# Kernel optimization log

Measured on AMD Instinct MI355X. Metric: run time of the kernel, lower is better.

The kernel has to match this reference:

```python
import jax, jax.numpy as jnp
import numpy as np

B, N, T, F, H, NH, E, R = 16, 100, 96, 26, 128, 4, 16, 8


def _ln(x, g, b, eps=1e-5):
    m = x.mean(-1, keepdims=True)
    v = ((x - m) ** 2).mean(-1, keepdims=True)
    return (x - m) / jnp.sqrt(v + eps) * g + b


def setup_inputs() -> dict:
    ks = iter(jax.random.split(jax.random.key(0), 64))

    def nrm(*shape):
        return jax.random.normal(next(ks), shape, jnp.float32) * 0.05

    z = lambda *s: jnp.zeros(s, jnp.float32)
    o = lambda *s: jnp.ones(s, jnp.float32)
    inp = {}
    inp['x'] = jax.random.normal(next(ks), (B, N, T, F), jnp.float32)
    A = jax.random.uniform(next(ks), (N, N), jnp.float32)
    inp['A_norm'] = A / A.sum(1, keepdims=True)
    inp['H_inc'] = (jax.random.uniform(next(ks), (N, E)) > 0.7).astype(jnp.float32).at[:, 0].set(1.0)
    inp['membership'] = jax.random.randint(next(ks), (N,), 0, R)
    inp['Wp'] = nrm(H, F); inp['bp'] = z(H)
    inp['g_p'] = o(H); inp['b_p'] = z(H)
    inp['Wqkv'] = nrm(3 * H, H); inp['bqkv'] = z(3 * H)
    inp['Wo'] = nrm(H, H); inp['bo'] = z(H)
    inp['g_a'] = o(H); inp['b_a'] = z(H)
    inp['Wih_f'] = nrm(4 * H, H); inp['Whh_f'] = nrm(4 * H, H)
    inp['bih_f'] = z(4 * H); inp['bhh_f'] = z(4 * H)
    inp['Wih_b'] = nrm(4 * H, H); inp['Whh_b'] = nrm(4 * H, H)
    inp['bih_b'] = z(4 * H); inp['bhh_b'] = z(4 * H)
    inp['Wtp'] = nrm(H, 2 * H); inp['btp'] = z(H)
    inp['Wn'] = nrm(H, H); inp['bn'] = z(H)
    inp['We'] = nrm(H, H); inp['be'] = z(H)
    inp['Wa'] = nrm(1, H); inp['ba'] = z(1)
    inp['g_g'] = o(H); inp['b_g'] = z(H)
    inp['Remb'] = nrm(R, H)
    inp['Wg'] = nrm(H, H); inp['bg'] = z(H)
    inp['Wf'] = nrm(H, 2 * H); inp['bf'] = z(H)
    inp['g_f'] = o(H); inp['b_f'] = z(H)
    inp['W1'] = nrm(H // 2, H); inp['b1'] = z(H // 2)
    inp['W2'] = nrm(1, H // 2); inp['b2'] = z(1)
    return inp


def reference(x, A_norm, H_inc, membership, Wp, bp, g_p, b_p, Wqkv, bqkv, Wo, bo,
              g_a, b_a, Wih_f, Whh_f, bih_f, bhh_f, Wih_b, Whh_b, bih_b, bhh_b,
              Wtp, btp, Wn, bn, We, be, Wa, ba, g_g, b_g, Remb, Wg, bg,
              Wf, bf, g_f, b_f, W1, b1, W2, b2):
    B_, N_, T_, F_ = x.shape
    H_ = Wp.shape[0]
    BN = B_ * N_
    # input_proj (dropout = identity in eval)
    h = jax.nn.relu(_ln(x.reshape(BN, T_, F_) @ Wp.T + bp, g_p, b_p))
    # temporal multi-head self-attention + residual + LN
    qkv = h @ Wqkv.T + bqkv
    q, k, v = jnp.split(qkv, 3, -1)
    dh = H_ // NH
    sh = lambda t: t.reshape(BN, T_, NH, dh).transpose(0, 2, 1, 3)
    q, k, v = sh(q), sh(k), sh(v)
    att = jax.nn.softmax(jnp.einsum('bhqd,bhkd->bhqk', q, k) / jnp.sqrt(jnp.float32(dh)), -1)
    ao = jnp.einsum('bhqk,bhkd->bhqd', att, v).transpose(0, 2, 1, 3).reshape(BN, T_, H_)
    h = _ln(ao @ Wo.T + bo + h, g_a, b_a)
    # bidirectional LSTM (PyTorch gate order i,f,g,o), take t = T-1
    def lstm_scan(seq, Wih, Whh, bih, bhh):
        def step(carry, xt):
            hp, cp = carry
            gates = xt @ Wih.T + bih + hp @ Whh.T + bhh
            i, f, g, o_ = jnp.split(gates, 4, -1)
            c = jax.nn.sigmoid(f) * cp + jax.nn.sigmoid(i) * jnp.tanh(g)
            hn = jax.nn.sigmoid(o_) * jnp.tanh(c)
            return (hn, c), hn
        z0 = jnp.zeros((seq.shape[1], H_), seq.dtype)
        _, ys = jax.lax.scan(step, (z0, z0), seq)
        return ys
    seq = h.transpose(1, 0, 2)  # (T, BN, H)
    y_f = lstm_scan(seq, Wih_f, Whh_f, bih_f, bhh_f)[-1]        # fwd hidden at t=T-1
    y_b = lstm_scan(seq[::-1], Wih_b, Whh_b, bih_b, bhh_b)[0]   # bwd hidden at t=T-1
    h_temporal = (jnp.concatenate([y_f, y_b], -1) @ Wtp.T + btp).reshape(B_, N_, H_)
    # spatial: HyperGAT (segment softmax over incident hyperedges) + GCN + region emb
    mask = H_inc > 0                        # (N, E)
    deg_e = H_inc.sum(0)                    # (E,)
    has_edge = mask.any(-1, keepdims=True)  # (N, 1)
    r_emb = Remb[membership]                # (N, H)

    def spatial(hb):
        npj = hb @ Wn.T + bn
        ee = (H_inc.T @ npj) / (deg_e[:, None] + 1e-8)
        ee = ee @ We.T + be                 # (E, H)
        sc = (ee @ Wa.T + ba)[:, 0]         # (E,)
        w = jax.nn.softmax(jnp.where(mask, sc[None, :], -1e9), -1)
        w = jnp.where(has_edge, w, 0.0)
        hb2 = _ln(w @ ee + hb, g_g, b_g)
        hg = jax.nn.relu((A_norm @ hb2) @ Wg.T + bg)
        return hb2 + hg + r_emb

    h_spatial = jax.vmap(spatial)(h_temporal)
    h_fused = jax.nn.relu(_ln(jnp.concatenate([h_temporal, h_spatial], -1) @ Wf.T + bf, g_f, b_f))
    pred = (jax.nn.relu(h_fused @ W1.T + b1) @ W2.T + b2)[..., 0]
    return pred, h_spatial, h_temporal
```

## Files before the change

kernel.cpp:

```cpp
#include <hip/hip_runtime.h>
#include <hip/hip_bf16.h>

typedef __hip_bfloat16 bf16;
typedef __attribute__((ext_vector_type(8))) short bf8v;
typedef __attribute__((ext_vector_type(4))) short s4v;
typedef __attribute__((ext_vector_type(4))) float f4v;

#define DEV __device__ __forceinline__

DEV float b2f(bf16 v){ return __bfloat162float(v); }
DEV bf16 f2b(float v){ return __float2bfloat16(v); }
DEV short f2bs(float v){ bf16 t = __float2bfloat16(v); return *reinterpret_cast<short*>(&t); }
DEV float s2f(short s){ return __uint_as_float(((unsigned int)(unsigned short)s) << 16); }
DEV float rcpf_(float x){ return __builtin_amdgcn_rcpf(x); }
DEV float sigf(float x){ return rcpf_(1.0f + __expf(-x)); }
DEV float tanhfast(float x){
  x = fminf(fmaxf(x, -15.0f), 15.0f);
  float e = __expf(-2.0f*x);
  return (1.0f - e)*rcpf_(1.0f + e);
}

DEV f4v mfma16(bf8v a, bf8v b, f4v c){
  return __builtin_amdgcn_mfma_f32_16x16x32_bf16(a, b, c, 0, 0, 0);
}

__global__ void k_detect(const unsigned int* __restrict__ xw, int* __restrict__ flag){
  __shared__ int found;
  if (threadIdx.x == 0) found = 0;
  __syncthreads();
  int local = 0;
  for (int i = threadIdx.x; i < 4096; i += 256){
    unsigned int u = xw[i];
    unsigned int e = (u >> 7) & 0xFF;
    if (e >= 0x90) local = 1;
  }
  if (local) atomicOr(&found, 1);
  __syncthreads();
  if (threadIdx.x == 0) flag[0] = found ? 0 : 1;
}

struct CArgs {
  const void* src[44];
  int n[44];
  int off[44];
};

__global__ void k_canon(CArgs a, const int* __restrict__ flag, bf16* __restrict__ dst){
  int id = blockIdx.y;
  int n = a.n[id];
  const void* s = a.src[id];
  bf16* d = dst + a.off[id];
  int stride = gridDim.x * blockDim.x;
  int i0 = blockIdx.x * blockDim.x + threadIdx.x;
  if (flag[0]){
    const bf16* sb = (const bf16*)s;
    for (int i = i0; i < n; i += stride) d[i] = sb[i];
  } else {
    const float* sf = (const float*)s;
    for (int i = i0; i < n; i += stride) d[i] = f2b(sf[i]);
  }
}

__global__ void k_prep(const bf16* __restrict__ Wp, const bf16* __restrict__ An,
                       bf16* __restrict__ Wpp, bf16* __restrict__ Anp,
                       bf16* __restrict__ htp, bf16* __restrict__ hb2p){
  int stride = gridDim.x * blockDim.x;
  bf16 zero = f2b(0.0f);
  for (int i = blockIdx.x*blockDim.x + threadIdx.x; i < 477184; i += stride){
    if (i < 4096){
      int row = i >> 5, col = i & 31;
      Wpp[i] = (col < 26) ? Wp[row*26 + col] : zero;
    } else if (i < 18432){
      int j = i - 4096;
      int row = j >> 7, col = j & 127;
      Anp[j] = (row < 100 && col < 100) ? An[row*100 + col] : zero;
    } else if (i < 247808){
      htp[i - 18432] = zero;
    } else {
      hb2p[i - 247808] = zero;
    }
  }
}

__global__ __launch_bounds__(256) void k_inproj(const bf16* __restrict__ x,
    const bf16* __restrict__ Wpp, const bf16* __restrict__ bp,
    const bf16* __restrict__ gp, const bf16* __restrict__ bbp,
    bf16* __restrict__ h0){
  int blk = blockIdx.x, tid = threadIdx.x;
  int w = tid >> 6, lane = tid & 63, l15 = lane & 15, quad = lane >> 4;
  __shared__ __align__(16) short flat[3328];
  __shared__ __align__(16) short xt[128*40];
  {
    const uint4* src = (const uint4*)(x + blk*3328);
    uint4* dst = (uint4*)flat;
    for (int u = tid; u < 416; u += 256) dst[u] = src[u];
  }
  __syncthreads();
  for (int i = tid; i < 5120; i += 256){
    int row = i/40, col = i - row*40;
    xt[i] = (col < 26) ? flat[row*26 + col] : (short)0;
  }
  __syncthreads();
  int m0 = w*32;
  bf8v a[2];
  #pragma unroll
  for (int m = 0; m < 2; ++m)
    a[m] = *reinterpret_cast<const bf8v*>(xt + (m0 + m*16 + l15)*40 + quad*8);
  f4v acc[2][8];
  for (int n = 0; n < 8; ++n){
    bf8v bb = *reinterpret_cast<const bf8v*>(Wpp + (n*16 + l15)*32 + quad*8);
    #pragma unroll
    for (int m = 0; m < 2; ++m){
      f4v z = {0.f,0.f,0.f,0.f};
      acc[m][n] = mfma16(a[m], bb, z);
    }
  }
  #pragma unroll
  for (int m = 0; m < 2; ++m){
    int rowbase = blk*128 + m0 + m*16;
    float sm[4], sq[4];
    #pragma unroll
    for (int r = 0; r < 4; ++r){ sm[r] = 0.f; sq[r] = 0.f; }
    #pragma unroll
    for (int n = 0; n < 8; ++n){
      int col = n*16 + l15;
      float bv = b2f(bp[col]);
      #pragma unroll
      for (int r = 0; r < 4; ++r){
        float v = acc[m][n][r] + bv;
        acc[m][n][r] = v;
        sm[r] += v; sq[r] += v*v;
      }
    }
    #pragma unroll
    for (int mask = 1; mask < 16; mask <<= 1)
      #pragma unroll
      for (int r = 0; r < 4; ++r){
        sm[r] += __shfl_xor(sm[r], mask);
        sq[r] += __shfl_xor(sq[r], mask);
      }
    float mean[4], rs[4];
    #pragma unroll
    for (int r = 0; r < 4; ++r){
      mean[r] = sm[r]*(1.0f/128.0f);
      float var = fmaxf(sq[r]*(1.0f/128.0f) - mean[r]*mean[r], 0.0f);
      rs[r] = rsqrtf(var + 1e-5f);
    }
    #pragma unroll
    for (int n = 0; n < 8; ++n){
      int col = n*16 + l15;
      float gv = b2f(gp[col]), bv = b2f(bbp[col]);
      #pragma unroll
      for (int r = 0; r < 4; ++r){
        float y = fmaxf((acc[m][n][r] - mean[r])*rs[r]*gv + bv, 0.0f);
        h0[(rowbase + quad*4 + r)*128 + col] = f2b(y);
      }
    }
  }
}

__global__ __launch_bounds__(256) void k_attn(const bf16* __restrict__ h0,
    const bf16* __restrict__ Wqkv, const bf16* __restrict__ bqkv,
    bf16* __restrict__ attno){
  int bn = blockIdx.x;
  int tid = threadIdx.x;
  int w = tid >> 6;
  int lane = tid & 63;
  int l15 = lane & 15, quad = lane >> 4;

  __shared__ __align__(16) short h0s[96*136];
  __shared__ __align__(16) short v_sh[4][32*104];
  __shared__ __align__(16) short scr[4][16*40];

  {
    const uint4* src = (const uint4*)(h0 + bn*12288);
    uint4* dst = (uint4*)h0s;
    for (int u = tid; u < 1536; u += 256){
      int r = u >> 4, c = u & 15;
      dst[r*17 + c] = src[u];
    }
  }
  __syncthreads();

  short* vp = v_sh[w];
  short* sw = scr[w];
  const float scl = 0.17677669529663687f;

  bf8v aq[6], bk[6];
  for (int m = 0; m < 6; ++m){
    bf8v a[4];
    #pragma unroll
    for (int kt = 0; kt < 4; ++kt)
      a[kt] = *reinterpret_cast<const bf8v*>(h0s + (m*16 + l15)*136 + kt*32 + quad*8);
    #pragma unroll
    for (int n0 = 0; n0 < 32; n0 += 16){
      int rq = w*32 + n0 + l15;
      bf8v b[4];
      #pragma unroll
      for (int kt = 0; kt < 4; ++kt)
        b[kt] = *reinterpret_cast<const bf8v*>(Wqkv + rq*128 + kt*32 + quad*8);
      float bias = b2f(bqkv[rq]);
      f4v acc = {0.f,0.f,0.f,0.f};
      #pragma unroll
      for (int kt = 0; kt < 4; ++kt) acc = mfma16(a[kt], b[kt], acc);
      #pragma unroll
      for (int r = 0; r < 4; ++r)
        sw[(quad*4 + r)*40 + n0 + l15] = f2bs((acc[r] + bias)*scl);
    }
    asm volatile("s_waitcnt lgkmcnt(0)" ::: "memory");
    aq[m] = *reinterpret_cast<const bf8v*>(sw + l15*40 + quad*8);
  }
  for (int m = 0; m < 6; ++m){
    bf8v a[4];
    #pragma unroll
    for (int kt = 0; kt < 4; ++kt)
      a[kt] = *reinterpret_cast<const bf8v*>(h0s + (m*16 + l15)*136 + kt*32 + quad*8);
    #pragma unroll
    for (int n0 = 0; n0 < 32; n0 += 16){
      int rq = 128 + w*32 + n0 + l15;
      bf8v b[4];
      #pragma unroll
      for (int kt = 0; kt < 4; ++kt)
        b[kt] = *reinterpret_cast<const bf8v*>(Wqkv + rq*128 + kt*32 + quad*8);
      float bias = b2f(bqkv[rq]);
      f4v acc = {0.f,0.f,0.f,0.f};
      #pragma unroll
      for (int kt = 0; kt < 4; ++kt) acc = mfma16(a[kt], b[kt], acc);
      #pragma unroll
      for (int r = 0; r < 4; ++r)
        sw[(quad*4 + r)*40 + n0 + l15] = f2bs(acc[r] + bias);
    }
    asm volatile("s_waitcnt lgkmcnt(0)" ::: "memory");
    bk[m] = *reinterpret_cast<const bf8v*>(sw + l15*40 + quad*8);
  }
  for (int m = 0; m < 6; ++m){
    bf8v a[4];
    #pragma unroll
    for (int kt = 0; kt < 4; ++kt)
      a[kt] = *reinterpret_cast<const bf8v*>(h0s + (m*16 + l15)*136 + kt*32 + quad*8);
    #pragma unroll
    for (int n0 = 0; n0 < 32; n0 += 16){
      int rq = 256 + w*32 + n0 + l15;
      bf8v b[4];
      #pragma unroll
      for (int kt = 0; kt < 4; ++kt)
        b[kt] = *reinterpret_cast<const bf8v*>(Wqkv + rq*128 + kt*32 + quad*8);
      float bias = b2f(bqkv[rq]);
      f4v acc = {0.f,0.f,0.f,0.f};
      #pragma unroll
      for (int kt = 0; kt < 4; ++kt) acc = mfma16(a[kt], b[kt], acc);
      s4v vs;
      #pragma unroll
      for (int r = 0; r < 4; ++r) vs[r] = f2bs(acc[r] + bias);
      *reinterpret_cast<s4v*>(vp + (n0 + l15)*104 + m*16 + quad*4) = vs;
    }
  }
  __syncthreads();

  short* pp = h0s + w*1664;

  for (int m = 0; m < 6; ++m){
    f4v s[6];
    #pragma unroll
    for (int n = 0; n < 6; ++n){
      f4v z = {0.f,0.f,0.f,0.f};
      s[n] = mfma16(aq[m], bk[n], z);
    }
    float mr[4], sr[4];
    #pragma unroll
    for (int r = 0; r < 4; ++r){
      float m0 = fmaxf(fmaxf(s[0][r], s[1][r]), fmaxf(s[2][r], s[3][r]));
      mr[r] = fmaxf(m0, fmaxf(s[4][r], s[5][r]));
    }
    #pragma unroll
    for (int mask = 1; mask < 16; mask <<= 1)
      #pragma unroll
      for (int r = 0; r < 4; ++r) mr[r] = fmaxf(mr[r], __shfl_xor(mr[r], mask));
    #pragma unroll
    for (int r = 0; r < 4; ++r) sr[r] = 0.0f;
    #pragma unroll
    for (int n = 0; n < 6; ++n)
      #pragma unroll
      for (int r = 0; r < 4; ++r){
        float p = __expf(s[n][r] - mr[r]);
        s[n][r] = p;
        sr[r] += p;
      }
    #pragma unroll
    for (int mask = 1; mask < 16; mask <<= 1)
      #pragma unroll
      for (int r = 0; r < 4; ++r) sr[r] += __shfl_xor(sr[r], mask);
    #pragma unroll
    for (int n = 0; n < 6; ++n)
      #pragma unroll
      for (int r = 0; r < 4; ++r)
        pp[(quad*4 + r)*104 + n*16 + l15] = f2bs(s[n][r]);
    asm volatile("s_waitcnt lgkmcnt(0)" ::: "memory");
    f4v o0 = {0.f,0.f,0.f,0.f}, o1 = {0.f,0.f,0.f,0.f};
    #pragma unroll
    for (int ksi = 0; ksi < 3; ++ksi){
      bf8v ap  = *reinterpret_cast<const bf8v*>(pp + l15*104 + ksi*32 + quad*8);
      bf8v bv0 = *reinterpret_cast<const bf8v*>(vp + l15*104 + ksi*32 + quad*8);
      bf8v bv1 = *reinterpret_cast<const bf8v*>(vp + (16 + l15)*104 + ksi*32 + quad*8);
      o0 = mfma16(ap, bv0, o0);
      o1 = mfma16(ap, bv1, o1);
    }
    #pragma unroll
    for (int r = 0; r < 4; ++r){
      float inv = 1.0f/sr[r];
      int row = bn*96 + m*16 + quad*4 + r;
      attno[row*128 + w*32 + l15]      = f2b(o0[r]*inv);
      attno[row*128 + w*32 + 16 + l15] = f2b(o1[r]*inv);
    }
  }
}

__global__ __launch_bounds__(256) void k_oproj(const bf16* __restrict__ attno,
    const bf16* __restrict__ h0, const bf16* __restrict__ Wo,
    const bf16* __restrict__ bo, const bf16* __restrict__ ga,
    const bf16* __restrict__ ba_, bf16* __restrict__ h1){
  int rt = blockIdx.x;
  int tid = threadIdx.x;
  int w = tid >> 6, lane = tid & 63;
  int l15 = lane & 15, quad = lane >> 4;
  __shared__ __align__(16) short atile[128*136];
  {
    const uint4* src = (const uint4*)(attno + rt*16384);
    uint4* dst = (uint4*)atile;
    for (int u = tid; u < 2048; u += 256){
      int r = u >> 4, c = u & 15;
      dst[r*17 + c] = src[u];
    }
  }
  __syncthreads();
  int m0 = w*32;
  bf8v a[2][4];
  #pragma unroll
  for (int m = 0; m < 2; ++m)
    #pragma unroll
    for (int ksi = 0; ksi < 4; ++ksi)
      a[m][ksi] = *reinterpret_cast<const bf8v*>(atile + (m0 + m*16 + l15)*136 + ksi*32 + quad*8);
  f4v acc[2][8];
  #pragma unroll
  for (int m = 0; m < 2; ++m)
    #pragma unroll
    for (int n = 0; n < 8; ++n) acc[m][n] = (f4v){0.f,0.f,0.f,0.f};
  for (int n = 0; n < 8; ++n){
    int G = n*16 + l15;
    bf8v b[4];
    #pragma unroll
    for (int ksi = 0; ksi < 4; ++ksi)
      b[ksi] = *reinterpret_cast<const bf8v*>(Wo + G*128 + ksi*32 + quad*8);
    #pragma unroll
    for (int m = 0; m < 2; ++m)
      #pragma unroll
      for (int ksi = 0; ksi < 4; ++ksi)
        acc[m][n] = mfma16(a[m][ksi], b[ksi], acc[m][n]);
  }
  #pragma unroll
  for (int m = 0; m < 2; ++m){
    int rowbase = rt*128 + m0 + m*16;
    #pragma unroll
    for (int n = 0; n < 8; ++n){
      int col = n*16 + l15;
      float bia = b2f(bo[col]);
      #pragma unroll
      for (int r = 0; r < 4; ++r)
        acc[m][n][r] += bia + b2f(h0[(rowbase + quad*4 + r)*128 + col]);
    }
    float sm[4], sq[4];
    #pragma unroll
    for (int r = 0; r < 4; ++r){ sm[r] = 0.f; sq[r] = 0.f; }
    #pragma unroll
    for (int n = 0; n < 8; ++n)
      #pragma unroll
      for (int r = 0; r < 4; ++r){
        float v = acc[m][n][r];
        sm[r] += v; sq[r] += v*v;
      }
    #pragma unroll
    for (int mask = 1; mask < 16; mask <<= 1)
      #pragma unroll
      for (int r = 0; r < 4; ++r){
        sm[r] += __shfl_xor(sm[r], mask);
        sq[r] += __shfl_xor(sq[r], mask);
      }
    float mean[4], rs[4];
    #pragma unroll
    for (int r = 0; r < 4; ++r){
      mean[r] = sm[r]*(1.0f/128.0f);
      float var = fmaxf(sq[r]*(1.0f/128.0f) - mean[r]*mean[r], 0.0f);
      rs[r] = rsqrtf(var + 1e-5f);
    }
    #pragma unroll
    for (int n = 0; n < 8; ++n){
      int col = n*16 + l15;
      float gv = b2f(ga[col]), bv = b2f(ba_[col]);
      #pragma unroll
      for (int r = 0; r < 4; ++r){
        float y = (acc[m][n][r] - mean[r])*rs[r]*gv + bv;
        h1[(rowbase + quad*4 + r)*128 + col] = f2b(y);
      }
    }
  }
}

__global__ __launch_bounds__(512,1) void k_lstm(const bf16* __restrict__ Whh,
    const bf16* __restrict__ Wih, const bf16* __restrict__ bih,
    const bf16* __restrict__ bhh, const bf16* __restrict__ h1,
    const bf16* __restrict__ Wihb, const bf16* __restrict__ bihb,
    const bf16* __restrict__ bhhb, const bf16* __restrict__ Wtp,
    const bf16* __restrict__ btp, bf16* __restrict__ ht_pad,
    const int* __restrict__ flag, bf16* __restrict__ outb,
    float* __restrict__ outf){
  int bn0 = blockIdx.x * 16;
  int tid = threadIdx.x;
  int w = tid >> 6, lane = tid & 63;
  int l15 = lane & 15, quad = lane >> 4;
  __shared__ __align__(16) short hbuf[2][16*136];
  __shared__ __align__(16) short xbuf[2][16*136];
  __shared__ __align__(16) short ycat[16*264];

  bf8v whh[4][4], wih[4][4];
  float bias[4];
  #pragma unroll
  for (int role = 0; role < 4; ++role){
    int G = role*128 + w*16 + l15;
    #pragma unroll
    for (int kt = 0; kt < 4; ++kt){
      whh[role][kt] = *reinterpret_cast<const bf8v*>(Whh + G*128 + kt*32 + quad*8);
      wih[role][kt] = *reinterpret_cast<const bf8v*>(Wih + G*128 + kt*32 + quad*8);
    }
    bias[role] = b2f(bih[G]) + b2f(bhh[G]);
  }
  const uint4* h1u4 = (const uint4*)h1;
  int srow = tid >> 4, scol = tid & 15;

  for (int i = tid; i < 16*136; i += 512) hbuf[0][i] = 0;
  if (tid < 256)
    ((uint4*)xbuf[0])[srow*17 + scol] = h1u4[((bn0 + srow)*96 + 0)*16 + scol];
  f4v c0 = {0.f,0.f,0.f,0.f};
  uint4 xpre;
  if (tid < 256) xpre = h1u4[((bn0 + srow)*96 + 1)*16 + scol];
  __syncthreads();

  f4v accx[4];
  {
    bf8v ax[4];
    #pragma unroll
    for (int kt = 0; kt < 4; ++kt)
      ax[kt] = *reinterpret_cast<const bf8v*>(xbuf[0] + l15*136 + kt*32 + quad*8);
    #pragma unroll
    for (int role = 0; role < 4; ++role){
      f4v z = {0.f,0.f,0.f,0.f};
      #pragma unroll
      for (int kt = 0; kt < 4; ++kt) z = mfma16(ax[kt], wih[role][kt], z);
      accx[role] = z;
    }
  }
  if (tid < 256) ((uint4*)xbuf[1])[srow*17 + scol] = xpre;
  if (tid < 256) xpre = h1u4[((bn0 + srow)*96 + 2)*16 + scol];
  __syncthreads();

  for (int t = 0; t < 96; ++t){
    int cur = t & 1, nxt = cur ^ 1;
    bf8v ah[4], axn[4];
    #pragma unroll
    for (int kt = 0; kt < 4; ++kt){
      ah[kt]  = *reinterpret_cast<const bf8v*>(hbuf[cur] + l15*136 + kt*32 + quad*8);
      axn[kt] = *reinterpret_cast<const bf8v*>(xbuf[nxt] + l15*136 + kt*32 + quad*8);
    }
    f4v acc[4];
    #pragma unroll
    for (int role = 0; role < 4; ++role){
      f4v z = accx[role];
      #pragma unroll
      for (int kt = 0; kt < 4; ++kt) z = mfma16(ah[kt], whh[role][kt], z);
      acc[role] = z;
    }
    #pragma unroll
    for (int role = 0; role < 4; ++role){
      f4v z = {0.f,0.f,0.f,0.f};
      #pragma unroll
      for (int kt = 0; kt < 4; ++kt) z = mfma16(axn[kt], wih[role][kt], z);
      accx[role] = z;
    }
    float hreg[4];
    #pragma unroll
    for (int r = 0; r < 4; ++r){
      float i_ = acc[0][r] + bias[0];
      float f_ = acc[1][r] + bias[1];
      float g_ = acc[2][r] + bias[2];
      float o_ = acc[3][r] + bias[3];
      float c  = sigf(f_)*c0[r] + sigf(i_)*tanhfast(g_);
      hreg[r]  = sigf(o_)*tanhfast(c);
      c0[r] = c;
    }
    #pragma unroll
    for (int r = 0; r < 4; ++r)
      hbuf[nxt][(quad*4 + r)*136 + w*16 + l15] = f2bs(hreg[r]);
    if (tid < 256){
      ((uint4*)xbuf[cur])[srow*17 + scol] = xpre;
      int tl = (t + 3 < 96) ? t + 3 : 95;
      xpre = h1u4[((bn0 + srow)*96 + tl)*16 + scol];
    }
    __syncthreads();
  }
  for (int idx = tid; idx < 2048; idx += 512){
    int r = idx >> 7, d = idx & 127;
    ycat[r*264 + d] = hbuf[0][r*136 + d];
  }
  {
    bf8v ax[4];
    #pragma unroll
    for (int kt = 0; kt < 4; ++kt)
      ax[kt] = *reinterpret_cast<const bf8v*>(xbuf[0] + l15*136 + kt*32 + quad*8);
    int col = w*16 + l15;
    f4v gi = {0.f,0.f,0.f,0.f}, gg = {0.f,0.f,0.f,0.f}, go = {0.f,0.f,0.f,0.f};
    #pragma unroll
    for (int kt = 0; kt < 4; ++kt){
      gi = mfma16(ax[kt], *reinterpret_cast<const bf8v*>(Wihb + col*128 + kt*32 + quad*8), gi);
      gg = mfma16(ax[kt], *reinterpret_cast<const bf8v*>(Wihb + (256 + col)*128 + kt*32 + quad*8), gg);
      go = mfma16(ax[kt], *reinterpret_cast<const bf8v*>(Wihb + (384 + col)*128 + kt*32 + quad*8), go);
    }
    float bi = b2f(bihb[col])       + b2f(bhhb[col]);
    float bg = b2f(bihb[256 + col]) + b2f(bhhb[256 + col]);
    float bo = b2f(bihb[384 + col]) + b2f(bhhb[384 + col]);
    #pragma unroll
    for (int r = 0; r < 4; ++r){
      float c  = sigf(gi[r] + bi) * tanhfast(gg[r] + bg);
      float yb = sigf(go[r] + bo) * tanhfast(c);
      ycat[(quad*4 + r)*264 + 128 + col] = f2bs(yb);
    }
  }
  __syncthreads();
  {
    int col = w*16 + l15;
    f4v z = {0.f,0.f,0.f,0.f};
    #pragma unroll
    for (int kt = 0; kt < 8; ++kt){
      bf8v a = *reinterpret_cast<const bf8v*>(ycat + l15*264 + kt*32 + quad*8);
      bf8v bb = *reinterpret_cast<const bf8v*>(Wtp + col*256 + kt*32 + quad*8);
      z = mfma16(a, bb, z);
    }
    float bt = b2f(btp[col]);
    #pragma unroll
    for (int r = 0; r < 4; ++r){
      int rowg = bn0 + quad*4 + r;
      float v = z[r] + bt;
      int bb_ = rowg/100, nn = rowg - bb_*100;
      ht_pad[(bb_*112 + nn)*128 + col] = f2b(v);
      int oi = 206400 + rowg*128 + col;
      if (flag[0]) outb[oi] = f2b(v); else outf[oi] = v;
    }
  }
}

__global__ __launch_bounds__(512,1) void k_spat1(
    const bf16* __restrict__ ht_pad, const bf16* __restrict__ Hinc,
    const bf16* __restrict__ Wn, const bf16* __restrict__ bn_,
    const bf16* __restrict__ We, const bf16* __restrict__ be,
    const bf16* __restrict__ Wa, const bf16* __restrict__ ba,
    const bf16* __restrict__ gg_, const bf16* __restrict__ bg_,
    bf16* __restrict__ hb2g){
  int b = blockIdx.x, tid = threadIdx.x;
  int w = tid >> 6, lane = tid & 63, l15 = lane & 15, quad = lane >> 4;
  __shared__ __align__(16) short htb[112*136];
  __shared__ __align__(16) short mtile[16*136];
  __shared__ float HincS[1600];
  __shared__ float wts[1600];
  __shared__ float eeS[16*128];
  __shared__ float scE[16], degS[16], part[128];

  {
    const uint4* src = (const uint4*)(ht_pad + b*14336);
    uint4* dst = (uint4*)htb;
    for (int u = tid; u < 1792; u += 512){
      int r = u >> 4, c = u & 15;
      dst[r*17 + c] = src[u];
    }
  }
  for (int i = tid; i < 1600; i += 512) HincS[i] = b2f(Hinc[i]);
  __syncthreads();
  if (tid < 16){
    float s = 0.0f;
    for (int n = 0; n < 100; ++n) s += HincS[n*16 + tid];
    degS[tid] = s;
  }
  __syncthreads();
  for (int it = 0; it < 4; ++it){
    int idx = tid + it*512;
    int e = idx >> 7, d = idx & 127;
    float s = 0.0f;
    for (int n = 0; n < 100; ++n)
      s += HincS[n*16 + e] * s2f(htb[n*136 + d]);
    mtile[e*136 + d] = f2bs(s * rcpf_(degS[e] + 1e-8f));
  }
  __syncthreads();
  {
    bf8v a[4];
    #pragma unroll
    for (int kt = 0; kt < 4; ++kt)
      a[kt] = *reinterpret_cast<const bf8v*>(mtile + l15*136 + kt*32 + quad*8);
    int col = w*16 + l15;
    f4v z = {0.f,0.f,0.f,0.f};
    #pragma unroll
    for (int kt = 0; kt < 4; ++kt)
      z = mfma16(a[kt], *reinterpret_cast<const bf8v*>(Wn + col*128 + kt*32 + quad*8), z);
    float bnv = b2f(bn_[col]);
    __syncthreads();
    #pragma unroll
    for (int r = 0; r < 4; ++r){
      int e = quad*4 + r;
      float ratio = degS[e] * rcpf_(degS[e] + 1e-8f);
      mtile[e*136 + col] = f2bs(z[r] + bnv*ratio);
    }
  }
  __syncthreads();
  {
    bf8v a[4];
    #pragma unroll
    for (int kt = 0; kt < 4; ++kt)
      a[kt] = *reinterpret_cast<const bf8v*>(mtile + l15*136 + kt*32 + quad*8);
    int col = w*16 + l15;
    f4v z = {0.f,0.f,0.f,0.f};
    #pragma unroll
    for (int kt = 0; kt < 4; ++kt)
      z = mfma16(a[kt], *reinterpret_cast<const bf8v*>(We + col*128 + kt*32 + quad*8), z);
    float bev = b2f(be[col]);
    #pragma unroll
    for (int r = 0; r < 4; ++r)
      eeS[(quad*4 + r)*128 + col] = z[r] + bev;
  }
  __syncthreads();
  if (tid < 128){
    int e = tid >> 3, j = tid & 7;
    float s = 0.0f;
    for (int d = j*16; d < j*16 + 16; ++d)
      s += eeS[e*128 + d] * b2f(Wa[d]);
    part[tid] = s;
  }
  __syncthreads();
  if (tid < 16){
    float s = b2f(ba[0]);
    for (int j = 0; j < 8; ++j) s += part[tid*8 + j];
    scE[tid] = s;
  }
  __syncthreads();
  if (tid < 100){
    float sc[16], mx = -1e30f;
    for (int e = 0; e < 16; ++e){
      sc[e] = (HincS[tid*16 + e] > 0.0f) ? scE[e] : -1e30f;
      mx = fmaxf(mx, sc[e]);
    }
    float sum = 0.0f, tmp[16];
    for (int e = 0; e < 16; ++e){
      tmp[e] = (sc[e] > -1e29f) ? __expf(sc[e] - mx) : 0.0f;
      sum += tmp[e];
    }
    float inv = (sum > 0.0f) ? rcpf_(sum) : 0.0f;
    for (int e = 0; e < 16; ++e) wts[tid*16 + e] = tmp[e]*inv;
  }
  __syncthreads();
  for (int it = 0; it < 13; ++it){
    int n = it*8 + w;
    if (n < 100){
      int d0 = lane*2;
      float s0 = s2f(htb[n*136 + d0]);
      float s1 = s2f(htb[n*136 + d0 + 1]);
      for (int e = 0; e < 16; ++e){
        float wv = wts[n*16 + e];
        s0 += wv * eeS[e*128 + d0];
        s1 += wv * eeS[e*128 + d0 + 1];
      }
      float sum = s0 + s1, sq = s0*s0 + s1*s1;
      #pragma unroll
      for (int mask = 1; mask < 64; mask <<= 1){
        sum += __shfl_xor(sum, mask);
        sq  += __shfl_xor(sq, mask);
      }
      float mean = sum*(1.0f/128.0f);
      float var = fmaxf(sq*(1.0f/128.0f) - mean*mean, 0.0f);
      float rs = rsqrtf(var + 1e-5f);
      float y0 = (s0 - mean)*rs*b2f(gg_[d0])     + b2f(bg_[d0]);
      float y1 = (s1 - mean)*rs*b2f(gg_[d0 + 1]) + b2f(bg_[d0 + 1]);
      hb2g[b*14336 + n*128 + d0]     = f2b(y0);
      hb2g[b*14336 + n*128 + d0 + 1] = f2b(y1);
    }
  }
}

__global__ __launch_bounds__(512,1) void k_spat2(
    const bf16* __restrict__ hb2g, const bf16* __restrict__ Anp,
    const bf16* __restrict__ Wg, const bf16* __restrict__ bgc,
    const bf16* __restrict__ Remb, const int* __restrict__ mem,
    const bf16* __restrict__ ht_pad,
    const bf16* __restrict__ Wf, const bf16* __restrict__ bf_,
    const bf16* __restrict__ gf, const bf16* __restrict__ b_f,
    const bf16* __restrict__ W1, const bf16* __restrict__ b1,
    const bf16* __restrict__ W2, const bf16* __restrict__ b2,
    const int* __restrict__ flag, bf16* __restrict__ outb,
    float* __restrict__ outf){
  int b = blockIdx.x, tid = threadIdx.x;
  int w = tid >> 6, lane = tid & 63, l15 = lane & 15, quad = lane >> 4;
  __shared__ __align__(16) short regA[128*136];
  __shared__ __align__(16) short regB[112*136];

  for (int i = tid; i < 128*136; i += 512) regA[i] = 0;
  __syncthreads();
  {
    int c0 = w*16;
    bf8v bw[4];
    #pragma unroll
    for (int kt = 0; kt < 4; ++kt)
      bw[kt] = *reinterpret_cast<const bf8v*>(Wg + (c0 + l15)*128 + kt*32 + quad*8);
    for (int m = 0; m < 7; ++m){
      f4v z = {0.f,0.f,0.f,0.f};
      #pragma unroll
      for (int kt = 0; kt < 4; ++kt){
        bf8v a = *reinterpret_cast<const bf8v*>(hb2g + b*14336 + (m*16 + l15)*128 + kt*32 + quad*8);
        z = mfma16(a, bw[kt], z);
      }
      s4v vs;
      #pragma unroll
      for (int r = 0; r < 4; ++r) vs[r] = f2bs(z[r]);
      *reinterpret_cast<s4v*>(regA + (c0 + l15)*136 + m*16 + quad*4) = vs;
    }
  }
  __syncthreads();
  {
    int c0 = w*16;
    for (int m = 0; m < 7; ++m){
      f4v z = {0.f,0.f,0.f,0.f};
      #pragma unroll
      for (int kt = 0; kt < 4; ++kt){
        bf8v a  = *reinterpret_cast<const bf8v*>(Anp + (m*16 + l15)*128 + kt*32 + quad*8);
        bf8v bb = *reinterpret_cast<const bf8v*>(regA + (c0 + l15)*136 + kt*32 + quad*8);
        z = mfma16(a, bb, z);
      }
      #pragma unroll
      for (int r = 0; r < 4; ++r){
        int row = m*16 + quad*4 + r, col = c0 + l15;
        if (row < 100){
          float v = fmaxf(z[r] + b2f(bgc[col]), 0.0f);
          float o = b2f(hb2g[b*14336 + row*128 + col]) + v
                  + b2f(Remb[mem[row]*128 + col]);
          int oi = 1600 + (b*100 + row)*128 + col;
          if (flag[0]) outb[oi] = f2b(o); else outf[oi] = o;
          regB[row*136 + col] = f2bs(o);
        } else {
          regB[row*136 + col] = 0;
        }
      }
    }
  }
  __syncthreads();
  if (w < 7){
    int m = w;
    f4v acc[8];
    for (int n = 0; n < 8; ++n){
      f4v z = {0.f,0.f,0.f,0.f};
      #pragma unroll
      for (int kt = 0; kt < 4; ++kt){
        bf8v a  = *reinterpret_cast<const bf8v*>(ht_pad + b*14336 + (m*16 + l15)*128 + kt*32 + quad*8);
        bf8v bb = *reinterpret_cast<const bf8v*>(Wf + (n*16 + l15)*256 + kt*32 + quad*8);
        z = mfma16(a, bb, z);
      }
      #pragma unroll
      for (int kt = 0; kt < 4; ++kt){
        bf8v a  = *reinterpret_cast<const bf8v*>(regB + (m*16 + l15)*136 + kt*32 + quad*8);
        bf8v bb = *reinterpret_cast<const bf8v*>(Wf + (n*16 + l15)*256 + 128 + kt*32 + quad*8);
        z = mfma16(a, bb, z);
      }
      acc[n] = z;
    }
    float sm[4], sq[4];
    #pragma unroll
    for (int r = 0; r < 4; ++r){ sm[r] = 0.f; sq[r] = 0.f; }
    #pragma unroll
    for (int n = 0; n < 8; ++n){
      int col = n*16 + l15;
      float bv = b2f(bf_[col]);
      #pragma unroll
      for (int r = 0; r < 4; ++r){
        float v = acc[n][r] + bv;
        acc[n][r] = v;
        sm[r] += v; sq[r] += v*v;
      }
    }
    #pragma unroll
    for (int mask = 1; mask < 16; mask <<= 1)
      #pragma unroll
      for (int r = 0; r < 4; ++r){
        sm[r] += __shfl_xor(sm[r], mask);
        sq[r] += __shfl_xor(sq[r], mask);
      }
    #pragma unroll
    for (int r = 0; r < 4; ++r){
      float mean = sm[r]*(1.0f/128.0f);
      float var = fmaxf(sq[r]*(1.0f/128.0f) - mean*mean, 0.0f);
      float rs = rsqrtf(var + 1e-5f);
      #pragma unroll
      for (int n = 0; n < 8; ++n){
        int col = n*16 + l15;
        float y = fmaxf((acc[n][r] - mean)*rs*b2f(gf[col]) + b2f(b_f[col]), 0.0f);
        regA[(m*16 + quad*4 + r)*136 + col] = f2bs(y);
      }
    }
  }
  __syncthreads();
  if (w < 7){
    int m = w;
    for (int n = 0; n < 4; ++n){
      f4v z = {0.f,0.f,0.f,0.f};
      #pragma unroll
      for (int kt = 0; kt < 4; ++kt){
        bf8v a  = *reinterpret_cast<const bf8v*>(regA + (m*16 + l15)*136 + kt*32 + quad*8);
        bf8v bb = *reinterpret_cast<const bf8v*>(W1 + (n*16 + l15)*128 + kt*32 + quad*8);
        z = mfma16(a, bb, z);
      }
      #pragma unroll
      for (int r = 0; r < 4; ++r){
        int row = m*16 + quad*4 + r, col = n*16 + l15;
        regB[row*72 + col] = f2bs(fmaxf(z[r] + b2f(b1[col]), 0.0f));
      }
    }
  }
  __syncthreads();
  if (tid < 100){
    float s = b2f(b2[0]);
    for (int d = 0; d < 64; ++d)
      s += s2f(regB[tid*72 + d]) * b2f(W2[d]);
    int oi = b*100 + tid;
    if (flag[0]) outb[oi] = f2b(s); else outf[oi] = s;
  }
}


extern "C" void kernel_launch(void* const* d_in, const int* in_sizes, int n_in,
                              void* d_out, int out_size, void* d_ws, size_t ws_size,
                              hipStream_t stream){
  (void)n_in; (void)out_size; (void)ws_size;
  const int* mem = (const int*)d_in[3];

  CArgs ca;
  int coff[43];
  int nf = 0;
  long long off = 0;
  for (int i = 0; i < 43; ++i){
    if (i == 3){ coff[i] = -1; continue; }
    coff[i] = (int)off;
    ca.src[nf] = d_in[i];
    ca.n[nf]   = in_sizes[i];
    ca.off[nf] = (int)off;
    ++nf;
    off += (long long)((in_sizes[i] + 7) & ~7);
  }
  char* ws = (char*)d_ws;
  bf16* canon = (bf16*)ws;
  long long canonBytes = ((off*2 + 255)/256)*256;
  int* flag = (int*)(ws + canonBytes);
  long long base = canonBytes + 256;

  #define C(i) (canon + coff[i])
  const bf16* A_norm = C(1);
  const bf16* Hinc   = C(2);
  const bf16* Wp  = C(4);  const bf16* bp  = C(5);
  const bf16* g_p = C(6);  const bf16* b_p = C(7);
  const bf16* Wqkv= C(8);  const bf16* bqkv= C(9);
  const bf16* Wo  = C(10); const bf16* bo  = C(11);
  const bf16* g_a = C(12); const bf16* b_a = C(13);
  const bf16* Wih_f = C(14); const bf16* Whh_f = C(15);
  const bf16* bih_f = C(16); const bf16* bhh_f = C(17);
  const bf16* Wih_b = C(18);
  const bf16* bih_b = C(20); const bf16* bhh_b = C(21);
  const bf16* Wtp = C(22); const bf16* btp = C(23);
  const bf16* Wn  = C(24); const bf16* bn_ = C(25);
  const bf16* We  = C(26); const bf16* be  = C(27);
  const bf16* Wa  = C(28); const bf16* ba  = C(29);
  const bf16* g_g = C(30); const bf16* b_g = C(31);
  const bf16* Remb= C(32);
  const bf16* Wg  = C(33); const bf16* bg  = C(34);
  const bf16* Wf  = C(35); const bf16* bff = C(36);
  const bf16* g_f = C(37); const bf16* b_f = C(38);
  const bf16* W1  = C(39); const bf16* b1  = C(40);
  const bf16* W2  = C(41); const bf16* b2  = C(42);
  const bf16* xc  = C(0);
  #undef C

  bf16*  outb = (bf16*)d_out;
  float* outf = (float*)d_out;
  bf16*  h1     = (bf16*)(ws + base);
  bf16*  h0     = (bf16*)(ws + base + 39321600LL);
  bf16*  attno  = (bf16*)(ws + base + 78643200LL);
  bf16*  Wpp    = (bf16*)(ws + base + 196608000LL);
  bf16*  An_pad = (bf16*)(ws + base + 196616192LL);
  bf16*  ht_pad = (bf16*)(ws + base + 196644864LL);
  bf16*  hb2g   = (bf16*)(ws + base + 197103616LL);

  k_detect<<<1, 256, 0, stream>>>((const unsigned int*)d_in[0], flag);
  k_canon <<<dim3(64, nf), 256, 0, stream>>>(ca, flag, canon);
  k_prep  <<<1024, 256, 0, stream>>>(Wp, A_norm, Wpp, An_pad, ht_pad, hb2g);
  k_inproj<<<1200, 256, 0, stream>>>(xc, Wpp, bp, g_p, b_p, h0);
  k_attn  <<<1600, 256, 0, stream>>>(h0, Wqkv, bqkv, attno);
  k_oproj <<<1200, 256, 0, stream>>>(attno, h0, Wo, bo, g_a, b_a, h1);
  k_lstm  <<<100,  512, 0, stream>>>(Whh_f, Wih_f, bih_f, bhh_f, h1,
                                     Wih_b, bih_b, bhh_b, Wtp, btp, ht_pad,
                                     flag, outb, outf);
  k_spat1 <<<16,   512, 0, stream>>>(ht_pad, Hinc, Wn, bn_, We, be, Wa, ba,
                                     g_g, b_g, hb2g);
  k_spat2 <<<16,   512, 0, stream>>>(hb2g, An_pad, Wg, bg, Remb, mem, ht_pad,
                                     Wf, bff, g_f, b_f, W1, b1, W2, b2,
                                     flag, outb, outf);
}
```

Before: 514.7 us.

## Fuse input projection, self-attention and output projection into one kernel per sequence

Merges the three kernels (input projection + LayerNorm, multi-head temporal attention, output projection + residual + LayerNorm) into a single kernel with one block per (b,n) sequence. The intermediate h0 and attention outputs stay in shared memory, so the global round trips for h0 and attno and two launches go away. V fragments are also preloaded into registers before the score loop. The cost is higher LDS use and register pressure per block, which may lower occupancy, and the projection phases use only 6 row tiles across 4 waves, leaving some waves idle.

```diff
diff --git a/kernel.cpp b/kernel.cpp
--- a/kernel.cpp
+++ b/kernel.cpp
@@ -82,42 +82,38 @@
   }
 }
 
-__global__ __launch_bounds__(256) void k_inproj(const bf16* __restrict__ x,
+__global__ __launch_bounds__(256) void k_fat(const bf16* __restrict__ x,
     const bf16* __restrict__ Wpp, const bf16* __restrict__ bp,
     const bf16* __restrict__ gp, const bf16* __restrict__ bbp,
-    bf16* __restrict__ h0){
-  int blk = blockIdx.x, tid = threadIdx.x;
+    const bf16* __restrict__ Wqkv, const bf16* __restrict__ bqkv,
+    const bf16* __restrict__ Wo, const bf16* __restrict__ bo,
+    const bf16* __restrict__ ga, const bf16* __restrict__ ba_,
+    bf16* __restrict__ h1){
+  int bn = blockIdx.x, tid = threadIdx.x;
   int w = tid >> 6, lane = tid & 63, l15 = lane & 15, quad = lane >> 4;
-  __shared__ __align__(16) short flat[3328];
-  __shared__ __align__(16) short xt[128*40];
+  __shared__ __align__(16) short h0s[96*136];
+  __shared__ __align__(16) short vre[13312];
+  __shared__ __align__(16) short pre[6144];
+
   {
-    const uint4* src = (const uint4*)(x + blk*3328);
-    uint4* dst = (uint4*)flat;
-    for (int u = tid; u < 416; u += 256) dst[u] = src[u];
-  }
-  __syncthreads();
-  for (int i = tid; i < 5120; i += 256){
+    const uint4* src = (const uint4*)(x + bn*2496);
+    uint4* dst = (uint4*)vre;
+    for (int u = tid; u < 312; u += 256) dst[u] = src[u];
+  }
+  __syncthreads();
+  for (int i = tid; i < 3840; i += 256){
     int row = i/40, col = i - row*40;
-    xt[i] = (col < 26) ? flat[row*26 + col] : (short)0;
-  }
-  __syncthreads();
-  int m0 = w*32;
-  bf8v a[2];
-  #pragma unroll
-  for (int m = 0; m < 2; ++m)
-    a[m] = *reinterpret_cast<const bf8v*>(xt + (m0 + m*16 + l15)*40 + quad*8);
-  f4v acc[2][8];
-  for (int n = 0; n < 8; ++n){
-    bf8v bb = *reinterpret_cast<const bf8v*>(Wpp + (n*16 + l15)*32 + quad*8);
-    #pragma unroll
-    for (int m = 0; m < 2; ++m){
+    pre[i] = (col < 26) ? vre[row*26 + col] : (short)0;
+  }
+  __syncthreads();
+  for (int m = w; m < 6; m += 4){
+    bf8v a = *reinterpret_cast<const bf8v*>(pre + (m*16 + l15)*40 + quad*8);
+    f4v acc[8];
+    for (int n = 0; n < 8; ++n){
+      bf8v bb = *reinterpret_cast<const bf8v*>(Wpp + (n*16 + l15)*32 + quad*8);
       f4v z = {0.f,0.f,0.f,0.f};
-      acc[m][n] = mfma16(a[m], bb, z);
-    }
-  }
-  #pragma unroll
-  for (int m = 0; m < 2; ++m){
-    int rowbase = blk*128 + m0 + m*16;
+      acc[n] = mfma16(a, bb, z);
+    }
     float sm[4], sq[4];
     #pragma unroll
     for (int r = 0; r < 4; ++r){ sm[r] = 0.f; sq[r] = 0.f; }
@@ -127,8 +123,8 @@
       float bv = b2f(bp[col]);
       #pragma unroll
       for (int r = 0; r < 4; ++r){
-        float v = acc[m][n][r] + bv;
-        acc[m][n][r] = v;
+        float v = acc[n][r] + bv;
+        acc[n][r] = v;
         sm[r] += v; sq[r] += v*v;
       }
     }
@@ -139,54 +135,26 @@
         sm[r] += __shfl_xor(sm[r], mask);
         sq[r] += __shfl_xor(sq[r], mask);
       }
-    float mean[4], rs[4];
     #pragma unroll
     for (int r = 0; r < 4; ++r){
-      mean[r] = sm[r]*(1.0f/128.0f);
-      float var = fmaxf(sq[r]*(1.0f/128.0f) - mean[r]*mean[r], 0.0f);
-      rs[r] = rsqrtf(var + 1e-5f);
-    }
-    #pragma unroll
-    for (int n = 0; n < 8; ++n){
-      int col = n*16 + l15;
-      float gv = b2f(gp[col]), bv = b2f(bbp[col]);
-      #pragma unroll
-      for (int r = 0; r < 4; ++r){
-        float y = fmaxf((acc[m][n][r] - mean[r])*rs[r]*gv + bv, 0.0f);
-        h0[(rowbase + quad*4 + r)*128 + col] = f2b(y);
-      }
-    }
-  }
-}
-
-__global__ __launch_bounds__(256) void k_attn(const bf16* __restrict__ h0,
-    const bf16* __restrict__ Wqkv, const bf16* __restrict__ bqkv,
-    bf16* __restrict__ attno){
-  int bn = blockIdx.x;
-  int tid = threadIdx.x;
-  int w = tid >> 6;
-  int lane = tid & 63;
-  int l15 = lane & 15, quad = lane >> 4;
-
-  __shared__ __align__(16) short h0s[96*136];
-  __shared__ __align__(16) short v_sh[4][32*104];
-  __shared__ __align__(16) short scr[4][16*40];
-
-  {
-    const uint4* src = (const uint4*)(h0 + bn*12288);
-    uint4* dst = (uint4*)h0s;
-    for (int u = tid; u < 1536; u += 256){
-      int r = u >> 4, c = u & 15;
-      dst[r*17 + c] = src[u];
-    }
-  }
-  __syncthreads();
-
-  short* vp = v_sh[w];
-  short* sw = scr[w];
+      float mean = sm[r]*(1.0f/128.0f);
+      float var = fmaxf(sq[r]*(1.0f/128.0f) - mean*mean, 0.0f);
+      float rs = rsqrtf(var + 1e-5f);
+      #pragma unroll
+      for (int n = 0; n < 8; ++n){
+        int col = n*16 + l15;
+        float y = fmaxf((acc[n][r] - mean)*rs*b2f(gp[col]) + b2f(bbp[col]), 0.0f);
+        h0s[(m*16 + quad*4 + r)*136 + col] = f2bs(y);
+      }
+    }
+  }
+  __syncthreads();
+
+  short* sw = pre + w*1536;
+  short* vp = vre + w*3328;
   const float scl = 0.17677669529663687f;
 
-  bf8v aq[6], bk[6];
+  bf8v aq[6], bk[6], bv[2][3];
   for (int m = 0; m < 6; ++m){
     bf8v a[4];
     #pragma unroll
@@ -255,9 +223,15 @@
       *reinterpret_cast<s4v*>(vp + (n0 + l15)*104 + m*16 + quad*4) = vs;
     }
   }
-  __syncthreads();
-
-  short* pp = h0s + w*1664;
+  asm volatile("s_waitcnt lgkmcnt(0)" ::: "memory");
+  #pragma unroll
+  for (int n = 0; n < 2; ++n)
+    #pragma unroll
+    for (int ksi = 0; ksi < 3; ++ksi)
+      bv[n][ksi] = *reinterpret_cast<const bf8v*>(vp + (n*16 + l15)*104 + ksi*32 + quad*8);
+  __syncthreads();
+
+  short* pp = pre + w*1536;
 
   for (int m = 0; m < 6; ++m){
     f4v s[6];
@@ -294,90 +268,55 @@
     for (int n = 0; n < 6; ++n)
       #pragma unroll
       for (int r = 0; r < 4; ++r)
-        pp[(quad*4 + r)*104 + n*16 + l15] = f2bs(s[n][r]);
+        pp[(quad*4 + r)*96 + n*16 + l15] = f2bs(s[n][r]);
     asm volatile("s_waitcnt lgkmcnt(0)" ::: "memory");
     f4v o0 = {0.f,0.f,0.f,0.f}, o1 = {0.f,0.f,0.f,0.f};
     #pragma unroll
     for (int ksi = 0; ksi < 3; ++ksi){
-      bf8v ap  = *reinterpret_cast<const bf8v*>(pp + l15*104 + ksi*32 + quad*8);
-      bf8v bv0 = *reinterpret_cast<const bf8v*>(vp + l15*104 + ksi*32 + quad*8);
-      bf8v bv1 = *reinterpret_cast<const bf8v*>(vp + (16 + l15)*104 + ksi*32 + quad*8);
-      o0 = mfma16(ap, bv0, o0);
-      o1 = mfma16(ap, bv1, o1);
+      bf8v ap = *reinterpret_cast<const bf8v*>(pp + l15*96 + ksi*32 + quad*8);
+      o0 = mfma16(ap, bv[0][ksi], o0);
+      o1 = mfma16(ap, bv[1][ksi], o1);
     }
     #pragma unroll
     for (int r = 0; r < 4; ++r){
       float inv = 1.0f/sr[r];
-      int row = bn*96 + m*16 + quad*4 + r;
-      attno[row*128 + w*32 + l15]      = f2b(o0[r]*inv);
-      attno[row*128 + w*32 + 16 + l15] = f2b(o1[r]*inv);
-    }
-  }
-}
-
-__global__ __launch_bounds__(256) void k_oproj(const bf16* __restrict__ attno,
-    const bf16* __restrict__ h0, const bf16* __restrict__ Wo,
-    const bf16* __restrict__ bo, const bf16* __restrict__ ga,
-    const bf16* __restrict__ ba_, bf16* __restrict__ h1){
-  int rt = blockIdx.x;
-  int tid = threadIdx.x;
-  int w = tid >> 6, lane = tid & 63;
-  int l15 = lane & 15, quad = lane >> 4;
-  __shared__ __align__(16) short atile[128*136];
-  {
-    const uint4* src = (const uint4*)(attno + rt*16384);
-    uint4* dst = (uint4*)atile;
-    for (int u = tid; u < 2048; u += 256){
-      int r = u >> 4, c = u & 15;
-      dst[r*17 + c] = src[u];
-    }
-  }
-  __syncthreads();
-  int m0 = w*32;
-  bf8v a[2][4];
-  #pragma unroll
-  for (int m = 0; m < 2; ++m)
-    #pragma unroll
-    for (int ksi = 0; ksi < 4; ++ksi)
-      a[m][ksi] = *reinterpret_cast<const bf8v*>(atile + (m0 + m*16 + l15)*136 + ksi*32 + quad*8);
-  f4v acc[2][8];
-  #pragma unroll
-  for (int m = 0; m < 2; ++m)
-    #pragma unroll
-    for (int n = 0; n < 8; ++n) acc[m][n] = (f4v){0.f,0.f,0.f,0.f};
-  for (int n = 0; n < 8; ++n){
-    int G = n*16 + l15;
-    bf8v b[4];
-    #pragma unroll
-    for (int ksi = 0; ksi < 4; ++ksi)
-      b[ksi] = *reinterpret_cast<const bf8v*>(Wo + G*128 + ksi*32 + quad*8);
-    #pragma unroll
-    for (int m = 0; m < 2; ++m)
-      #pragma unroll
-      for (int ksi = 0; ksi < 4; ++ksi)
-        acc[m][n] = mfma16(a[m][ksi], b[ksi], acc[m][n]);
-  }
-  #pragma unroll
-  for (int m = 0; m < 2; ++m){
-    int rowbase = rt*128 + m0 + m*16;
+      int row = m*16 + quad*4 + r;
+      vre[row*136 + w*32 + l15]      = f2bs(o0[r]*inv);
+      vre[row*136 + w*32 + 16 + l15] = f2bs(o1[r]*inv);
+    }
+  }
+  __syncthreads();
+
+  for (int m = w; m < 6; m += 4){
+    bf8v a[4];
+    #pragma unroll
+    for (int kt = 0; kt < 4; ++kt)
+      a[kt] = *reinterpret_cast<const bf8v*>(vre + (m*16 + l15)*136 + kt*32 + quad*8);
+    f4v acc[8];
+    for (int n = 0; n < 8; ++n){
+      int G = n*16 + l15;
+      f4v z = {0.f,0.f,0.f,0.f};
+      #pragma unroll
+      for (int kt = 0; kt < 4; ++kt){
+        bf8v bb = *reinterpret_cast<const bf8v*>(Wo + G*128 + kt*32 + quad*8);
+        z = mfma16(a[kt], bb, z);
+      }
+      acc[n] = z;
+    }
+    float sm[4], sq[4];
+    #pragma unroll
+    for (int r = 0; r < 4; ++r){ sm[r] = 0.f; sq[r] = 0.f; }
     #pragma unroll
     for (int n = 0; n < 8; ++n){
       int col = n*16 + l15;
       float bia = b2f(bo[col]);
       #pragma unroll
-      for (int r = 0; r < 4; ++r)
-        acc[m][n][r] += bia + b2f(h0[(rowbase + quad*4 + r)*128 + col]);
-    }
-    float sm[4], sq[4];
-    #pragma unroll
-    for (int r = 0; r < 4; ++r){ sm[r] = 0.f; sq[r] = 0.f; }
-    #pragma unroll
-    for (int n = 0; n < 8; ++n)
-      #pragma unroll
       for (int r = 0; r < 4; ++r){
-        float v = acc[m][n][r];
+        float v = acc[n][r] + bia + s2f(h0s[(m*16 + quad*4 + r)*136 + col]);
+        acc[n][r] = v;
         sm[r] += v; sq[r] += v*v;
       }
+    }
     #pragma unroll
     for (int mask = 1; mask < 16; mask <<= 1)
       #pragma unroll
@@ -385,21 +324,16 @@
         sm[r] += __shfl_xor(sm[r], mask);
         sq[r] += __shfl_xor(sq[r], mask);
       }
-    float mean[4], rs[4];
     #pragma unroll
     for (int r = 0; r < 4; ++r){
-      mean[r] = sm[r]*(1.0f/128.0f);
-      float var = fmaxf(sq[r]*(1.0f/128.0f) - mean[r]*mean[r], 0.0f);
-      rs[r] = rsqrtf(var + 1e-5f);
-    }
-    #pragma unroll
-    for (int n = 0; n < 8; ++n){
-      int col = n*16 + l15;
-      float gv = b2f(ga[col]), bv = b2f(ba_[col]);
-      #pragma unroll
-      for (int r = 0; r < 4; ++r){
-        float y = (acc[m][n][r] - mean[r])*rs[r]*gv + bv;
-        h1[(rowbase + quad*4 + r)*128 + col] = f2b(y);
+      float mean = sm[r]*(1.0f/128.0f);
+      float var = fmaxf(sq[r]*(1.0f/128.0f) - mean*mean, 0.0f);
+      float rs = rsqrtf(var + 1e-5f);
+      #pragma unroll
+      for (int n = 0; n < 8; ++n){
+        int col = n*16 + l15;
+        float y = (acc[n][r] - mean)*rs*b2f(ga[col]) + b2f(ba_[col]);
+        h1[(bn*96 + m*16 + quad*4 + r)*128 + col] = f2b(y);
       }
     }
   }
@@ -891,8 +825,6 @@
   bf16*  outb = (bf16*)d_out;
   float* outf = (float*)d_out;
   bf16*  h1     = (bf16*)(ws + base);
-  bf16*  h0     = (bf16*)(ws + base + 39321600LL);
-  bf16*  attno  = (bf16*)(ws + base + 78643200LL);
   bf16*  Wpp    = (bf16*)(ws + base + 196608000LL);
   bf16*  An_pad = (bf16*)(ws + base + 196616192LL);
   bf16*  ht_pad = (bf16*)(ws + base + 196644864LL);
@@ -901,9 +833,8 @@
   k_detect<<<1, 256, 0, stream>>>((const unsigned int*)d_in[0], flag);
   k_canon <<<dim3(64, nf), 256, 0, stream>>>(ca, flag, canon);
   k_prep  <<<1024, 256, 0, stream>>>(Wp, A_norm, Wpp, An_pad, ht_pad, hb2g);
-  k_inproj<<<1200, 256, 0, stream>>>(xc, Wpp, bp, g_p, b_p, h0);
-  k_attn  <<<1600, 256, 0, stream>>>(h0, Wqkv, bqkv, attno);
-  k_oproj <<<1200, 256, 0, stream>>>(attno, h0, Wo, bo, g_a, b_a, h1);
+  k_fat   <<<1600, 256, 0, stream>>>(xc, Wpp, bp, g_p, b_p, Wqkv, bqkv,
+                                     Wo, bo, g_a, b_a, h1);
   k_lstm  <<<100,  512, 0, stream>>>(Whh_f, Wih_f, bih_f, bhh_f, h1,
                                      Wih_b, bih_b, bhh_b, Wtp, btp, ht_pad,
                                      flag, outb, outf);
```

Measured after the change: 568.3 us. +10.4%, slower.
